# Performance work log

Measured on AMD Instinct MI355X. Metric: run time of the kernel, lower is better.

The kernel has to match this reference:

```python
import jax, jax.numpy as jnp
import numpy as np

N, E, IN, H, HEADS, L, OUT = 4096, 262144, 64, 128, 4, 2, 2
DH = H // HEADS  # 32, per-head dim for both GAT and global MHA
BN_EPS = 1e-5
NEG_SLOPE = 0.2  # GATConv leaky_relu default


def setup_inputs() -> dict:
    key = jax.random.key(0)
    ks = iter(jax.random.split(key, 32))
    rn = lambda shape, s: jax.random.normal(next(ks), shape, jnp.float32) * s
    return {
        "x": rn((N, IN), 1.0),
        "edge_index": jax.random.randint(next(ks), (2, E), 0, N),
        "w_in": rn((H, IN), IN ** -0.5),
        "b_in": rn((H,), 0.02),
        "w_gat": rn((L, H, H), H ** -0.5),
        "att_src": rn((L, HEADS, DH), 0.1),
        "att_dst": rn((L, HEADS, DH), 0.1),
        "b_gat": rn((L, H), 0.02),
        "w_qkv": rn((L, 3 * H, H), H ** -0.5),
        "b_qkv": rn((L, 3 * H), 0.02),
        "w_o": rn((L, H, H), H ** -0.5),
        "b_o": rn((L, H), 0.02),
        "bn_gamma": 1.0 + rn((L, 3, H), 0.05),
        "bn_beta": rn((L, 3, H), 0.05),
        "w1": rn((L, 2 * H, H), H ** -0.5),
        "b1": rn((L, 2 * H), 0.02),
        "w2": rn((L, H, 2 * H), (2 * H) ** -0.5),
        "b2": rn((L, H), 0.02),
        "w_out": rn((OUT, H), H ** -0.5),
        "b_out": rn((OUT,), 0.02),
    }


def _bn(h, g, b):
    # eval-mode BatchNorm1d with running_mean=0, running_var=1
    return h * (g / jnp.sqrt(1.0 + BN_EPS)) + b


def _gat(x, src, dst, w, a_src, a_dst, bias):
    # GATConv(hidden, hidden//heads, heads=HEADS, add_self_loops=False), concat=True
    xp = (x @ w.T).reshape(N, HEADS, DH)                  # [N, HEADS, DH]
    al_s = jnp.einsum('nhd,hd->nh', xp, a_src)            # [N, HEADS]
    al_d = jnp.einsum('nhd,hd->nh', xp, a_dst)
    logit = al_s[src] + al_d[dst]                         # [E, HEADS]
    logit = jnp.where(logit >= 0, logit, NEG_SLOPE * logit)
    m = jax.ops.segment_max(logit, dst, num_segments=N)   # scatter-softmax over dst
    m = jnp.where(jnp.isfinite(m), m, 0.0)
    e = jnp.exp(logit - m[dst])
    denom = jax.ops.segment_sum(e, dst, num_segments=N)
    alpha = e / (denom[dst] + 1e-16)
    out = jax.ops.segment_sum(alpha[:, :, None] * xp[src], dst, num_segments=N)
    return out.reshape(N, H) + bias


def _mha(x, wqkv, bqkv, wo, bo):
    # torch.nn.MultiheadAttention self-attention over all N nodes (one graph)
    qkv = x @ wqkv.T + bqkv
    q, k, v = jnp.split(qkv, 3, axis=-1)
    q = q.reshape(N, HEADS, DH)
    k = k.reshape(N, HEADS, DH)
    v = v.reshape(N, HEADS, DH)
    scores = jnp.einsum('nhd,mhd->hnm', q, k) / jnp.sqrt(jnp.float32(DH))
    attn = jax.nn.softmax(scores, axis=-1)
    out = jnp.einsum('hnm,mhd->nhd', attn, v).reshape(N, H)
    return out @ wo.T + bo


def reference(x, edge_index, w_in, b_in, w_gat, att_src, att_dst, b_gat,
              w_qkv, b_qkv, w_o, b_o, bn_gamma, bn_beta,
              w1, b1, w2, b2, w_out, b_out):
    src, dst = edge_index[0], edge_index[1]
    h = jax.nn.relu(x @ w_in.T + b_in)
    for l in range(L):
        # GPSConv: local GAT branch (dropout inactive in eval)
        h_loc = _gat(h, src, dst, w_gat[l], att_src[l], att_dst[l], b_gat[l]) + h
        h_loc = _bn(h_loc, bn_gamma[l, 0], bn_beta[l, 0])
        # GPSConv: global attention branch
        h_att = _mha(h, w_qkv[l], b_qkv[l], w_o[l], b_o[l]) + h
        h_att = _bn(h_att, bn_gamma[l, 1], bn_beta[l, 1])
        out = h_loc + h_att
        mlp = jax.nn.relu(out @ w1[l].T + b1[l]) @ w2[l].T + b2[l]
        out = _bn(out + mlp, bn_gamma[l, 2], bn_beta[l, 2])
        # GPSRiskModel residual + relu (dropout inactive in eval)
        h = jax.nn.relu(out + h)
    return h @ w_out.T + b_out
```

## Files before the change

### kernel.cpp

```cpp
#include <hip/hip_runtime.h>

#define NN 4096
#define EE 262144
#define INF_ 64
#define HH 128
#define HEADS 4
#define DH 32
#define LL 2
#define NH (NN * HH)
#define KSPLIT 16
#define L2E 1.4426950408889634f

typedef unsigned short u16;
typedef unsigned int u32;
using bf16x8 = __attribute__((ext_vector_type(8))) short;
using f32x4 = __attribute__((ext_vector_type(4))) float;

__device__ __forceinline__ float bf2f(u16 v) { return __uint_as_float(((u32)v) << 16); }
__device__ __forceinline__ u16 f2bf(float f) {
    u32 u = __float_as_uint(f);
    u32 r = (u + 0x7fffu + ((u >> 16) & 1u)) >> 16;
    return (u16)r;
}
__device__ __forceinline__ u32 encf(float f) {
    u32 b = __float_as_uint(f);
    return (b & 0x80000000u) ? ~b : (b | 0x80000000u);
}
__device__ __forceinline__ float decf(u32 u) {
    u32 b = (u & 0x80000000u) ? (u & 0x7fffffffu) : ~u;
    return __uint_as_float(b);
}

__global__ __launch_bounds__(256) void k_detect(const u16* __restrict__ x, int* __restrict__ flag,
                                                int* __restrict__ cnt, u32* __restrict__ gmax) {
    int t = threadIdx.x;
    for (int i = t; i < NN; i += 256) cnt[i] = 0;
    if (t < 16) gmax[t] = 0;
    __shared__ int cs[256];
    u16 v = x[2 * t];
    int e = (v >> 7) & 0xFF;
    cs[t] = (e >= 100 && e <= 140) ? 1 : 0;
    __syncthreads();
    for (int s = 128; s > 0; s >>= 1) {
        if (t < s) cs[t] += cs[t + s];
        __syncthreads();
    }
    if (t == 0) *flag = (cs[0] >= 128) ? 1 : 0;
}

#define MAXSEG 16
struct SegF { const void* src[MAXSEG]; int dst[MAXSEG]; int n[MAXSEG]; int cnt; };
struct SegB { const void* src[8]; u16* dst[8]; u16* dst2[8]; int n[8]; int cnt; };
__global__ __launch_bounds__(256) void k_prep(SegF SF, float* __restrict__ W, SegB SB,
                                              const int* __restrict__ flag,
                                              const int* __restrict__ dst, int* __restrict__ cnt) {
    int bid = blockIdx.x, t = threadIdx.x;
    if (bid < 96) {
        int seg = bid >> 3, bx = bid & 7;
        if (seg >= SF.cnt) return;
        int n = SF.n[seg];
        float* d = W + SF.dst[seg];
        const void* s = SF.src[seg];
        int f = *flag;
        for (int i = bx * 256 + t; i < n; i += 8 * 256)
            d[i] = f ? bf2f(((const u16*)s)[i]) : ((const float*)s)[i];
    } else if (bid < 992) {
        int b2 = bid - 96;
        int seg = b2 >> 7, bx = b2 & 127;
        if (seg >= SB.cnt) return;
        int f = *flag;
        u16* d = SB.dst[seg];
        u16* d2 = SB.dst2[seg];
        if (f && !d2) return;
        int n = SB.n[seg];
        const void* s = SB.src[seg];
        for (int i = bx * 256 + t; i < n; i += 128 * 256) {
            if (d2) {
                float v = f ? bf2f(((const u16*)s)[i]) : ((const float*)s)[i];
                u16 h = f2bf(v);
                d[i] = h;
                d2[i] = f2bf(v - bf2f(h));
            } else {
                d[i] = f2bf(((const float*)s)[i]);
            }
        }
    } else {
        int e = (bid - 992) * 256 + t;
        if (e < EE) atomicAdd(&cnt[dst[e]], 1);
    }
}

__global__ __launch_bounds__(256) void k_scan(const int* __restrict__ cnt, int* __restrict__ rowstart,
                                              int* __restrict__ cursor) {
    __shared__ int part[256];
    int t = threadIdx.x;
    int loc[16];
    int s = 0;
#pragma unroll
    for (int i = 0; i < 16; ++i) { loc[i] = s; s += cnt[t * 16 + i]; }
    part[t] = s;
    __syncthreads();
    for (int off = 1; off < 256; off <<= 1) {
        int v = part[t];
        int a = (t >= off) ? part[t - off] : 0;
        __syncthreads();
        part[t] = v + a;
        __syncthreads();
    }
    int base = (t == 0) ? 0 : part[t - 1];
#pragma unroll
    for (int i = 0; i < 16; ++i) {
        rowstart[t * 16 + i] = base + loc[i];
        cursor[t * 16 + i] = base + loc[i];
    }
}
__global__ void k_scatter(const int* __restrict__ src, const int* __restrict__ dst,
                          int* __restrict__ cursor, int* __restrict__ esrc) {
    int e = blockIdx.x * blockDim.x + threadIdx.x;
    if (e < EE) {
        int d = dst[e];
        int p = atomicAdd(&cursor[d], 1);
        esrc[p] = src[e];
    }
}

__global__ __launch_bounds__(128) void k_mgemm(const u16* __restrict__ Ahi, const u16* __restrict__ Alo,
                                               const u16* __restrict__ Wc, const u16* __restrict__ Wd,
                                               const int* __restrict__ flag,
                                               const float* __restrict__ bias,
                                               float* __restrict__ outf, u16* __restrict__ outb16,
                                               u16* __restrict__ outhi, u16* __restrict__ outlo,
                                               int K, int J, int relu) {
    const u16* Wb = (*flag) ? Wd : Wc;
    int wave = threadIdx.x >> 6, lane = threadIdx.x & 63;
    int grp = lane >> 4, lcol = lane & 15;
    int m0 = blockIdx.x * 32 + wave * 16;
    int j0 = blockIdx.y * 64;
    f32x4 acc[4];
#pragma unroll
    for (int s = 0; s < 4; ++s) acc[s] = (f32x4){0.f, 0.f, 0.f, 0.f};
    const u16* ah = Ahi + (size_t)(m0 + lcol) * K + grp * 8;
    const u16* al = Alo + (size_t)(m0 + lcol) * K + grp * 8;
    const u16* wb = Wb + (size_t)(j0 + lcol) * K + grp * 8;
    for (int k = 0; k < K; k += 32) {
        bf16x8 va = *(const bf16x8*)(ah + k);
        bf16x8 vl = *(const bf16x8*)(al + k);
#pragma unroll
        for (int s = 0; s < 4; ++s) {
            bf16x8 vw = *(const bf16x8*)(wb + (size_t)s * 16 * K + k);
            acc[s] = __builtin_amdgcn_mfma_f32_16x16x32_bf16(va, vw, acc[s], 0, 0, 0);
            acc[s] = __builtin_amdgcn_mfma_f32_16x16x32_bf16(vl, vw, acc[s], 0, 0, 0);
        }
    }
#pragma unroll
    for (int s = 0; s < 4; ++s) {
        int col = j0 + s * 16 + lcol;
        float bs = bias ? bias[col] : 0.f;
#pragma unroll
        for (int r = 0; r < 4; ++r) {
            float v = acc[s][r] + bs;
            if (relu) v = fmaxf(v, 0.f);
            size_t idx = (size_t)(m0 + grp * 4 + r) * J + col;
            if (outf) outf[idx] = v;
            if (outb16) outb16[idx] = f2bf(v);
            if (outhi) {
                u16 hv = f2bf(v);
                outhi[idx] = hv;
                outlo[idx] = f2bf(v - bf2f(hv));
            }
        }
    }
}

__global__ __launch_bounds__(128) void k_gemm_gq(const u16* __restrict__ Ahi, const u16* __restrict__ Alo,
                                                 const u16* __restrict__ wgatc, const u16* __restrict__ wgatd,
                                                 const u16* __restrict__ wqkvc, const u16* __restrict__ wqkvd,
                                                 const int* __restrict__ flag,
                                                 const float* __restrict__ bqkv,
                                                 u16* __restrict__ xpb, u16* __restrict__ qkvb) {
    int wave = threadIdx.x >> 6, lane = threadIdx.x & 63;
    int grp = lane >> 4, lcol = lane & 15;
    int m0 = blockIdx.x * 32 + wave * 16;
    int jb = blockIdx.y;
    int j0 = jb * 64;
    int f = *flag;
    const u16* wgat = f ? wgatd : wgatc;
    const u16* wqkv = f ? wqkvd : wqkvc;
    const u16* Wb = (jb < 2) ? (wgat + (size_t)j0 * HH) : (wqkv + (size_t)(j0 - 128) * HH);
    f32x4 acc[4];
#pragma unroll
    for (int s = 0; s < 4; ++s) acc[s] = (f32x4){0.f, 0.f, 0.f, 0.f};
    const u16* ah = Ahi + (size_t)(m0 + lcol) * HH + grp * 8;
    const u16* al = Alo + (size_t)(m0 + lcol) * HH + grp * 8;
    const u16* wb = Wb + (size_t)lcol * HH + grp * 8;
    for (int k = 0; k < HH; k += 32) {
        bf16x8 va = *(const bf16x8*)(ah + k);
        bf16x8 vl = *(const bf16x8*)(al + k);
#pragma unroll
        for (int s = 0; s < 4; ++s) {
            bf16x8 vw = *(const bf16x8*)(wb + (size_t)s * 16 * HH + k);
            acc[s] = __builtin_amdgcn_mfma_f32_16x16x32_bf16(va, vw, acc[s], 0, 0, 0);
            acc[s] = __builtin_amdgcn_mfma_f32_16x16x32_bf16(vl, vw, acc[s], 0, 0, 0);
        }
    }
    if (jb < 2) {
#pragma unroll
        for (int s = 0; s < 4; ++s) {
            int col = j0 + s * 16 + lcol;
#pragma unroll
            for (int r = 0; r < 4; ++r)
                xpb[(size_t)(m0 + grp * 4 + r) * HH + col] = f2bf(acc[s][r]);
        }
    } else {
#pragma unroll
        for (int s = 0; s < 4; ++s) {
            int colq = j0 - 128 + s * 16 + lcol;
            float bs = bqkv[colq];
#pragma unroll
            for (int r = 0; r < 4; ++r)
                qkvb[(size_t)(m0 + grp * 4 + r) * 384 + colq] = f2bf(acc[s][r] + bs);
        }
    }
}

__global__ __launch_bounds__(128) void k_gemm_wo(const u16* __restrict__ Ahi, const u16* __restrict__ Alo,
                                                 const u16* __restrict__ Wc, const u16* __restrict__ Wd,
                                                 const int* __restrict__ flag,
                                                 const float* __restrict__ bias,
                                                 const float* __restrict__ gatb, const float* __restrict__ hbuf,
                                                 const float* __restrict__ bgat, const float* __restrict__ gam,
                                                 const float* __restrict__ bet,
                                                 float* __restrict__ outb, u16* __restrict__ ohi,
                                                 u16* __restrict__ olo) {
    const u16* Wb = (*flag) ? Wd : Wc;
    int wave = threadIdx.x >> 6, lane = threadIdx.x & 63;
    int grp = lane >> 4, lcol = lane & 15;
    int m0 = blockIdx.x * 32 + wave * 16;
    int j0 = blockIdx.y * 64;
    f32x4 acc[4];
#pragma unroll
    for (int s = 0; s < 4; ++s) acc[s] = (f32x4){0.f, 0.f, 0.f, 0.f};
    const u16* ah = Ahi + (size_t)(m0 + lcol) * HH + grp * 8;
    const u16* al = Alo + (size_t)(m0 + lcol) * HH + grp * 8;
    const u16* wb = Wb + (size_t)(j0 + lcol) * HH + grp * 8;
    for (int k = 0; k < HH; k += 32) {
        bf16x8 va = *(const bf16x8*)(ah + k);
        bf16x8 vl = *(const bf16x8*)(al + k);
#pragma unroll
        for (int s = 0; s < 4; ++s) {
            bf16x8 vw = *(const bf16x8*)(wb + (size_t)s * 16 * HH + k);
            acc[s] = __builtin_amdgcn_mfma_f32_16x16x32_bf16(va, vw, acc[s], 0, 0, 0);
            acc[s] = __builtin_amdgcn_mfma_f32_16x16x32_bf16(vl, vw, acc[s], 0, 0, 0);
        }
    }
    float rs = rsqrtf(1.00001f);
#pragma unroll
    for (int s = 0; s < 4; ++s) {
        int col = j0 + s * 16 + lcol;
        float bs = bias[col];
        float g0 = gam[col] * rs, b0 = bet[col];
        float g1 = gam[HH + col] * rs, b1 = bet[HH + col];
        float bg = bgat[col];
#pragma unroll
        for (int r = 0; r < 4; ++r) {
            size_t idx = (size_t)(m0 + grp * 4 + r) * HH + col;
            float proj = acc[s][r] + bs;
            float hv = hbuf[idx];
            float hl = g0 * (gatb[idx] + bg + hv) + b0;
            float ha = g1 * (proj + hv) + b1;
            float v = hl + ha;
            outb[idx] = v;
            u16 hb = f2bf(v);
            ohi[idx] = hb;
            olo[idx] = f2bf(v - bf2f(hb));
        }
    }
}

__global__ __launch_bounds__(128) void k_gemm_w2(const u16* __restrict__ Ahi, const u16* __restrict__ Alo,
                                                 const u16* __restrict__ Wc, const u16* __restrict__ Wd,
                                                 const int* __restrict__ flag,
                                                 const float* __restrict__ bias,
                                                 const float* __restrict__ outb, const float* __restrict__ gam2,
                                                 const float* __restrict__ bet2,
                                                 float* __restrict__ hbuf, u16* __restrict__ hhi,
                                                 u16* __restrict__ hlo) {
    const u16* Wb = (*flag) ? Wd : Wc;
    int wave = threadIdx.x >> 6, lane = threadIdx.x & 63;
    int grp = lane >> 4, lcol = lane & 15;
    int m0 = blockIdx.x * 32 + wave * 16;
    int j0 = blockIdx.y * 64;
    const int K = 2 * HH;
    f32x4 acc[4];
#pragma unroll
    for (int s = 0; s < 4; ++s) acc[s] = (f32x4){0.f, 0.f, 0.f, 0.f};
    const u16* ah = Ahi + (size_t)(m0 + lcol) * K + grp * 8;
    const u16* al = Alo + (size_t)(m0 + lcol) * K + grp * 8;
    const u16* wb = Wb + (size_t)(j0 + lcol) * K + grp * 8;
    for (int k = 0; k < K; k += 32) {
        bf16x8 va = *(const bf16x8*)(ah + k);
        bf16x8 vl = *(const bf16x8*)(al + k);
#pragma unroll
        for (int s = 0; s < 4; ++s) {
            bf16x8 vw = *(const bf16x8*)(wb + (size_t)s * 16 * K + k);
            acc[s] = __builtin_amdgcn_mfma_f32_16x16x32_bf16(va, vw, acc[s], 0, 0, 0);
            acc[s] = __builtin_amdgcn_mfma_f32_16x16x32_bf16(vl, vw, acc[s], 0, 0, 0);
        }
    }
    float rs = rsqrtf(1.00001f);
#pragma unroll
    for (int s = 0; s < 4; ++s) {
        int col = j0 + s * 16 + lcol;
        float bs = bias[col];
        float g2 = gam2[col] * rs, b2 = bet2[col];
#pragma unroll
        for (int r = 0; r < 4; ++r) {
            size_t idx = (size_t)(m0 + grp * 4 + r) * HH + col;
            float mlpo = acc[s][r] + bs;
            float o2 = g2 * (outb[idx] + mlpo) + b2;
            float v = fmaxf(o2 + hbuf[idx], 0.f);
            hbuf[idx] = v;
            u16 hb = f2bf(v);
            hhi[idx] = hb;
            hlo[idx] = f2bf(v - bf2f(hb));
        }
    }
}

__global__ __launch_bounds__(256) void k_splitlog(const u16* __restrict__ qkvb,
                                                  float* __restrict__ PM, float* __restrict__ PL,
                                                  u16* __restrict__ PO,
                                                  const u16* __restrict__ xpb,
                                                  const float* __restrict__ asrc,
                                                  const float* __restrict__ adst,
                                                  float* __restrict__ als, float* __restrict__ ald,
                                                  u32* __restrict__ gmax) {
    __shared__ __align__(16) u16 Klds[64][40];
    __shared__ __align__(16) u32 Vlds[32][40];
    __shared__ __align__(16) u16 Plds[4][32][36];

    if (blockIdx.x >= 2048) {
        float* red = (float*)&Klds[0][0];
        int t = (blockIdx.x - 2048) * 256 + threadIdx.x;
        int n = t >> 2, hh = t & 3;
        const u16* xr = xpb + (size_t)n * HH + hh * DH;
        float s1 = 0.f, s2 = 0.f;
#pragma unroll
        for (int d = 0; d < DH; ++d) {
            float v = bf2f(xr[d]);
            s1 += v * asrc[hh * DH + d];
            s2 += v * adst[hh * DH + d];
        }
        als[t] = s1;
        ald[t] = s2;
        int lt = threadIdx.x;
        red[lt] = s1;
        __syncthreads();
        for (int off = 128; off >= 4; off >>= 1) {
            if (lt < off) red[lt] = fmaxf(red[lt], red[lt + off]);
            __syncthreads();
        }
        if (lt < 4) atomicMax(&gmax[lt], encf(red[lt]));
        __syncthreads();
        red[lt] = s2;
        __syncthreads();
        for (int off = 128; off >= 4; off >>= 1) {
            if (lt < off) red[lt] = fmaxf(red[lt], red[lt + off]);
            __syncthreads();
        }
        if (lt < 4) atomicMax(&gmax[4 + lt], encf(red[lt]));
        return;
    }

    const float C1 = 0.17677669529663687f * L2E;
    int head = blockIdx.x & 3;
    int qt = (blockIdx.x >> 2) & 31;
    int ks = blockIdx.x >> 7;
    int tid = threadIdx.x;
    int wave = tid >> 6, lane = tid & 63;
    int grp = lane >> 4, lcol = lane & 15;

    int qrow0 = qt * 128 + wave * 32;
    bf16x8 aQ0 = *(const bf16x8*)(qkvb + (size_t)(qrow0 + lcol) * 384 + head * 32 + grp * 8);
    bf16x8 aQ1 = *(const bf16x8*)(qkvb + (size_t)(qrow0 + 16 + lcol) * 384 + head * 32 + grp * 8);

    short onev = (lcol == 0) ? (short)0x3F80 : (short)0;
    bf16x8 bOne = {onev, onev, onev, onev, onev, onev, onev, onev};

    f32x4 oc00 = {0.f, 0.f, 0.f, 0.f}, oc01 = {0.f, 0.f, 0.f, 0.f};
    f32x4 oc10 = {0.f, 0.f, 0.f, 0.f}, oc11 = {0.f, 0.f, 0.f, 0.f};
    f32x4 ol0 = {0.f, 0.f, 0.f, 0.f}, ol1 = {0.f, 0.f, 0.f, 0.f};
    float msh = -INFINITY;

    int isK = (tid < 128);
    int st = tid & 127;
    int skey = st >> 1, shalf = (st & 1) * 16;
    int vj = st & 15, vc = (st >> 4) & 1, dgrp = st >> 5;
    const u16* kptr = qkvb + 128 + head * 32 + shalf;
    const u16* vptr = qkvb + 256 + head * 32 + dgrp * 8;
    int vk0 = vc * 32 + vj;
    int vk1 = vc * 32 + 16 + vj;

    int kt0 = ks * (NN / KSPLIT);
    bf16x8 r0, r1;
    if (isK) {
        r0 = *(const bf16x8*)(kptr + (size_t)(kt0 + skey) * 384);
        r1 = *(const bf16x8*)(kptr + (size_t)(kt0 + skey) * 384 + 8);
    } else {
        r0 = *(const bf16x8*)(vptr + (size_t)(kt0 + vk0) * 384);
        r1 = *(const bf16x8*)(vptr + (size_t)(kt0 + vk1) * 384);
    }

    const int NT = (NN / KSPLIT) / 64;
    for (int t = 0; t < NT; ++t) {
        if (isK) {
            *(bf16x8*)(&Klds[skey][shalf]) = r0;
            *(bf16x8*)(&Klds[skey][shalf + 8]) = r1;
        } else {
#pragma unroll
            for (int j = 0; j < 8; ++j)
                Vlds[dgrp * 8 + j][vc * 20 + vj] = (u32)(u16)r0[j] | ((u32)(u16)r1[j] << 16);
        }
        __syncthreads();
        if (t + 1 < NT) {
            int kn = kt0 + (t + 1) * 64;
            if (isK) {
                r0 = *(const bf16x8*)(kptr + (size_t)(kn + skey) * 384);
                r1 = *(const bf16x8*)(kptr + (size_t)(kn + skey) * 384 + 8);
            } else {
                r0 = *(const bf16x8*)(vptr + (size_t)(kn + vk0) * 384);
                r1 = *(const bf16x8*)(vptr + (size_t)(kn + vk1) * 384);
            }
        }
        f32x4 sc0[4], sc1[4];
        f32x4 zero = {0.f, 0.f, 0.f, 0.f};
#pragma unroll
        for (int s = 0; s < 4; ++s) {
            bf16x8 bK = *(const bf16x8*)(&Klds[s * 16 + lcol][grp * 8]);
            sc0[s] = __builtin_amdgcn_mfma_f32_16x16x32_bf16(aQ0, bK, zero, 0, 0, 0);
            sc1[s] = __builtin_amdgcn_mfma_f32_16x16x32_bf16(aQ1, bK, zero, 0, 0, 0);
        }
        float mymax = sc0[0][0];
#pragma unroll
        for (int s = 0; s < 4; ++s)
#pragma unroll
            for (int r = 0; r < 4; ++r) {
                mymax = fmaxf(mymax, sc0[s][r]);
                mymax = fmaxf(mymax, sc1[s][r]);
            }
        mymax = fmaxf(mymax, __shfl_xor(mymax, 1));
        mymax = fmaxf(mymax, __shfl_xor(mymax, 2));
        mymax = fmaxf(mymax, __shfl_xor(mymax, 4));
        mymax = fmaxf(mymax, __shfl_xor(mymax, 8));
        float mnew = fmaxf(msh, mymax * C1);
        float cc = __builtin_exp2f(msh - mnew);
        msh = mnew;
        oc00 *= cc; oc01 *= cc; ol0 *= cc;
        oc10 *= cc; oc11 *= cc; ol1 *= cc;
#pragma unroll
        for (int c2 = 0; c2 < 2; ++c2) {
#pragma unroll
            for (int r = 0; r < 4; ++r) {
                float p0 = __builtin_exp2f(__builtin_fmaf(sc0[2 * c2][r], C1, -mnew));
                float p1 = __builtin_exp2f(__builtin_fmaf(sc0[2 * c2 + 1][r], C1, -mnew));
                *(u32*)(&Plds[wave][grp * 4 + r][2 * lcol]) =
                    __builtin_amdgcn_perm(__float_as_uint(p1), __float_as_uint(p0), 0x07060302u);
                float q0 = __builtin_exp2f(__builtin_fmaf(sc1[2 * c2][r], C1, -mnew));
                float q1 = __builtin_exp2f(__builtin_fmaf(sc1[2 * c2 + 1][r], C1, -mnew));
                *(u32*)(&Plds[wave][16 + grp * 4 + r][2 * lcol]) =
                    __builtin_amdgcn_perm(__float_as_uint(q1), __float_as_uint(q0), 0x07060302u);
            }
            bf16x8 aP0 = *(const bf16x8*)(&Plds[wave][lcol][grp * 8]);
            bf16x8 aP1 = *(const bf16x8*)(&Plds[wave][16 + lcol][grp * 8]);
            bf16x8 bV0 = *(const bf16x8*)(&Vlds[lcol][c2 * 20 + grp * 4]);
            bf16x8 bV1 = *(const bf16x8*)(&Vlds[16 + lcol][c2 * 20 + grp * 4]);
            oc00 = __builtin_amdgcn_mfma_f32_16x16x32_bf16(aP0, bV0, oc00, 0, 0, 0);
            oc01 = __builtin_amdgcn_mfma_f32_16x16x32_bf16(aP0, bV1, oc01, 0, 0, 0);
            ol0 = __builtin_amdgcn_mfma_f32_16x16x32_bf16(aP0, bOne, ol0, 0, 0, 0);
            oc10 = __builtin_amdgcn_mfma_f32_16x16x32_bf16(aP1, bV0, oc10, 0, 0, 0);
            oc11 = __builtin_amdgcn_mfma_f32_16x16x32_bf16(aP1, bV1, oc11, 0, 0, 0);
            ol1 = __builtin_amdgcn_mfma_f32_16x16x32_bf16(aP1, bOne, ol1, 0, 0, 0);
        }
        __syncthreads();
    }
#pragma unroll
    for (int r = 0; r < 4; ++r) {
        int row0 = qrow0 + grp * 4 + r;
        size_t b0 = ((size_t)row0 * HEADS + head) * KSPLIT + ks;
        PO[b0 * 32 + lcol] = f2bf(oc00[r]);
        PO[b0 * 32 + 16 + lcol] = f2bf(oc01[r]);
        int row1 = row0 + 16;
        size_t b1 = ((size_t)row1 * HEADS + head) * KSPLIT + ks;
        PO[b1 * 32 + lcol] = f2bf(oc10[r]);
        PO[b1 * 32 + 16 + lcol] = f2bf(oc11[r]);
        if (lcol == 0) {
            PM[b0] = msh;
            PL[b0] = ol0[r];
            PM[b1] = msh;
            PL[b1] = ol1[r];
        }
    }
}

#define GCHUNK 256
__global__ __launch_bounds__(128) void k_gatcomb(const int* __restrict__ esrc, const int* __restrict__ rowstart,
                                                 const int* __restrict__ cnt, const float* __restrict__ als,
                                                 const float* __restrict__ ald, const u16* __restrict__ xpb,
                                                 float* __restrict__ gatout, const u32* __restrict__ gmax,
                                                 const float* __restrict__ PM, const float* __restrict__ PL,
                                                 const u16* __restrict__ PO, u16* __restrict__ atthi,
                                                 u16* __restrict__ attlo) {
    __shared__ float red[512];
    __shared__ float elds[GCHUNK * 4];
    __shared__ int slds[GCHUNK];
    int t = threadIdx.x;

    if (blockIdx.x >= NN) {
        int n2 = blockIdx.x - NN;
        float* wn = red;
        if (t < 64) {
            int head = t >> 4, ks = t & 15;
            size_t b = ((size_t)n2 * HEADS + head) * KSPLIT + ks;
            float pm = PM[b];
            float m = pm;
#pragma unroll
            for (int off = 1; off < 16; off <<= 1) m = fmaxf(m, __shfl_xor(m, off));
            float w = __builtin_exp2f(pm - m);
            float lw = PL[b] * w;
#pragma unroll
            for (int off = 1; off < 16; off <<= 1) lw += __shfl_xor(lw, off);
            wn[t] = w / lw;
        }
        __syncthreads();
        int head = t >> 5, dim = t & 31;
        size_t b0 = ((size_t)n2 * HEADS + head) * KSPLIT;
        float o = 0.f;
#pragma unroll
        for (int k = 0; k < KSPLIT; ++k)
            o += wn[head * 16 + k] * bf2f(PO[(b0 + k) * 32 + dim]);
        size_t idx = (size_t)n2 * HH + t;
        u16 h = f2bf(o);
        atthi[idx] = h;
        attlo[idx] = f2bf(o - bf2f(h));
        return;
    }

    int n = blockIdx.x;
    int base = rowstart[n], c = cnt[n];
    float4 adv = ((const float4*)ald)[n];
    float ad[4] = {adv.x, adv.y, adv.z, adv.w};
    float M2[4];
#pragma unroll
    for (int h = 0; h < 4; ++h) {
        float bound = decf(gmax[h]) + decf(gmax[4 + h]);
        float M = bound >= 0.f ? bound : 0.2f * bound;
        M2[h] = M * L2E;
    }
    float dsum[4] = {0.f, 0.f, 0.f, 0.f};
    float acc = 0.f;
    int ht = t >> 5;
    for (int ch = 0; ch < c; ch += GCHUNK) {
        int cn = min(GCHUNK, c - ch);
        __syncthreads();
        for (int i = t; i < cn; i += 128) {
            int s = esrc[base + ch + i];
            slds[i] = s;
            float4 as = ((const float4*)als)[s];
            float lg, e;
            lg = as.x + ad[0]; lg = lg >= 0.f ? lg : 0.2f * lg; e = __builtin_exp2f(lg * L2E - M2[0]); elds[i * 4 + 0] = e; dsum[0] += e;
            lg = as.y + ad[1]; lg = lg >= 0.f ? lg : 0.2f * lg; e = __builtin_exp2f(lg * L2E - M2[1]); elds[i * 4 + 1] = e; dsum[1] += e;
            lg = as.z + ad[2]; lg = lg >= 0.f ? lg : 0.2f * lg; e = __builtin_exp2f(lg * L2E - M2[2]); elds[i * 4 + 2] = e; dsum[2] += e;
            lg = as.w + ad[3]; lg = lg >= 0.f ? lg : 0.2f * lg; e = __builtin_exp2f(lg * L2E - M2[3]); elds[i * 4 + 3] = e; dsum[3] += e;
        }
        __syncthreads();
        int i = 0;
        for (; i + 4 <= cn; i += 4) {
            int s0 = slds[i], s1 = slds[i + 1], s2 = slds[i + 2], s3 = slds[i + 3];
            float x0 = bf2f(xpb[(size_t)s0 * HH + t]);
            float x1 = bf2f(xpb[(size_t)s1 * HH + t]);
            float x2 = bf2f(xpb[(size_t)s2 * HH + t]);
            float x3 = bf2f(xpb[(size_t)s3 * HH + t]);
            acc += elds[i * 4 + ht] * x0 + elds[(i + 1) * 4 + ht] * x1;
            acc += elds[(i + 2) * 4 + ht] * x2 + elds[(i + 3) * 4 + ht] * x3;
        }
        for (; i < cn; ++i) acc += elds[i * 4 + ht] * bf2f(xpb[(size_t)slds[i] * HH + t]);
    }
    __syncthreads();
#pragma unroll
    for (int h = 0; h < 4; ++h) red[h * 128 + t] = dsum[h];
    __syncthreads();
    for (int s2 = 64; s2 > 0; s2 >>= 1) {
        if (t < s2) {
#pragma unroll
            for (int h = 0; h < 4; ++h)
                red[h * 128 + t] += red[h * 128 + t + s2];
        }
        __syncthreads();
    }
    float inv = 1.f / (red[ht * 128] + 1e-16f);
    gatout[(size_t)n * HH + t] = acc * inv;
}

__global__ __launch_bounds__(64) void k_out(const float* __restrict__ h, const float* __restrict__ w,
                                            const float* __restrict__ b, void* __restrict__ yout,
                                            const int* __restrict__ flag) {
    int n = blockIdx.x, l = threadIdx.x;
    float a0 = 0.f, a1 = 0.f;
    for (int k = l; k < HH; k += 64) {
        float hv = h[(size_t)n * HH + k];
        a0 += hv * w[k];
        a1 += hv * w[HH + k];
    }
#pragma unroll
    for (int off = 32; off > 0; off >>= 1) {
        a0 += __shfl_xor(a0, off);
        a1 += __shfl_xor(a1, off);
    }
    if (l == 0) {
        float o0 = a0 + b[0], o1 = a1 + b[1];
        if (*flag) {
            u16* y = (u16*)yout;
            y[n * 2 + 0] = f2bf(o0);
            y[n * 2 + 1] = f2bf(o1);
        } else {
            float* y = (float*)yout;
            y[n * 2 + 0] = o0;
            y[n * 2 + 1] = o1;
        }
    }
}

extern "C" void kernel_launch(void* const* d_in, const int* in_sizes, int n_in,
                              void* d_out, int out_size, void* d_ws, size_t ws_size,
                              hipStream_t stream) {
    float* W = (float*)d_ws;
    size_t o = 0;
    auto take = [&](size_t n) { size_t r = o; o += n; return r; };
    size_t pb_in = take(HH);
    size_t pattS = take(LL * HEADS * DH);
    size_t pattD = take(LL * HEADS * DH);
    size_t pb_gat = take(LL * HH);
    size_t pb_qkv = take(LL * 3 * HH);
    size_t pb_o  = take(LL * HH);
    size_t pbn_g = take(LL * 3 * HH);
    size_t pbn_b = take(LL * 3 * HH);
    size_t pb1   = take(LL * 2 * HH);
    size_t pb2   = take(LL * HH);
    size_t pw_out = take(2 * HH);
    size_t pb_out = take(2);
    auto takeb = [&](size_t nu16) { size_t r = o; o += (nu16 + 1) / 2; return r; };
    size_t bw_in  = takeb(HH * INF_);
    size_t bw_gat = takeb(LL * HH * HH);
    size_t bw_qkv = takeb(LL * 3 * HH * HH);
    size_t bw_o   = takeb(LL * HH * HH);
    size_t bw1    = takeb(LL * 2 * HH * HH);
    size_t bw2    = takeb(LL * HH * 2 * HH);
    o = (o + 127) & ~(size_t)127;
    size_t ohbuf = take(NH);
    size_t ogat  = take(NH);
    size_t otmp  = take(NH);
    size_t oals  = take(NN * HEADS);
    size_t oald  = take(NN * HEADS);
    size_t opm   = take(NN * HEADS * KSPLIT);
    size_t opl   = take(NN * HEADS * KSPLIT);
    size_t opo   = takeb((size_t)NN * HEADS * KSPLIT * 32);
    size_t oqkvb = takeb(NN * 384);
    size_t oxpb  = takeb(NH);
    size_t oxhi  = takeb(NN * INF_);
    size_t oxlo  = takeb(NN * INF_);
    size_t ohhi  = takeb(NH);
    size_t ohlo  = takeb(NH);
    size_t oahi  = takeb(NH);
    size_t oalo  = takeb(NH);
    size_t oohi  = takeb(NH);
    size_t oolo  = takeb(NH);
    size_t omhi  = takeb(NN * 2 * HH);
    size_t omlo  = takeb(NN * 2 * HH);
    int* ibase    = (int*)(W + o);
    int* iflag    = ibase;
    int* cnt      = ibase + 64;
    int* rowstart = cnt + NN;
    int* cursor   = rowstart + NN;
    int* esrc     = cursor + NN;
    u32* gmax     = (u32*)(esrc + EE);

    float* hbuf = W + ohbuf;
    float* gatb = W + ogat;
    float* tmp  = W + otmp;
    float* als  = W + oals;
    float* ald  = W + oald;
    float* pmb  = W + opm;
    float* plb  = W + opl;
    u16* pob  = (u16*)(W + opo);
    u16* qkvb = (u16*)(W + oqkvb);
    u16* xpb  = (u16*)(W + oxpb);
    u16* xhi = (u16*)(W + oxhi), *xlo = (u16*)(W + oxlo);
    u16* hhi = (u16*)(W + ohhi), *hlo = (u16*)(W + ohlo);
    u16* ahi = (u16*)(W + oahi), *alo = (u16*)(W + oalo);
    u16* ohi = (u16*)(W + oohi), *olo = (u16*)(W + oolo);
    u16* mhi = (u16*)(W + omhi), *mlo = (u16*)(W + omlo);

    const int* src = (const int*)d_in[1];
    const int* dst = (const int*)d_in[1] + EE;
    const u16* dw_in  = (const u16*)d_in[2];
    const u16* dw_gat = (const u16*)d_in[4];
    const u16* dw_qkv = (const u16*)d_in[8];
    const u16* dw_o   = (const u16*)d_in[10];
    const u16* dw1    = (const u16*)d_in[14];
    const u16* dw2    = (const u16*)d_in[16];

    k_detect<<<1, 256, 0, stream>>>((const u16*)d_in[0], iflag, cnt, gmax);

    SegF SF = {};
    int nf = 0;
    auto addf = [&](int idx, size_t off, int n) { SF.src[nf] = d_in[idx]; SF.dst[nf] = (int)off; SF.n[nf] = n; ++nf; };
    addf(3, pb_in, HH);
    addf(5, pattS, LL * HEADS * DH);
    addf(6, pattD, LL * HEADS * DH);
    addf(7, pb_gat, LL * HH);
    addf(9, pb_qkv, LL * 3 * HH);
    addf(11, pb_o, LL * HH);
    addf(12, pbn_g, LL * 3 * HH);
    addf(13, pbn_b, LL * 3 * HH);
    addf(15, pb1, LL * 2 * HH);
    addf(17, pb2, LL * HH);
    addf(18, pw_out, 2 * HH);
    addf(19, pb_out, 2);
    SF.cnt = nf;

    SegB SB = {};
    int nb = 0;
    auto addb = [&](int idx, size_t off, int n, u16* d2) {
        SB.src[nb] = d_in[idx]; SB.dst[nb] = (u16*)(W + off); SB.dst2[nb] = d2; SB.n[nb] = n; ++nb;
    };
    addb(2, bw_in, HH * INF_, nullptr);
    addb(4, bw_gat, LL * HH * HH, nullptr);
    addb(8, bw_qkv, LL * 3 * HH * HH, nullptr);
    addb(10, bw_o, LL * HH * HH, nullptr);
    addb(14, bw1, LL * 2 * HH * HH, nullptr);
    addb(16, bw2, LL * HH * 2 * HH, nullptr);
    SB.src[nb] = d_in[0]; SB.dst[nb] = xhi; SB.dst2[nb] = xlo; SB.n[nb] = NN * INF_; ++nb;
    SB.cnt = nb;

    k_prep<<<2016, 256, 0, stream>>>(SF, W, SB, iflag, dst, cnt);

    k_scan<<<1, 256, 0, stream>>>(cnt, rowstart, cursor);
    k_scatter<<<EE / 256, 256, 0, stream>>>(src, dst, cursor, esrc);

    k_mgemm<<<dim3(NN / 32, HH / 64), 128, 0, stream>>>(xhi, xlo, (u16*)(W + bw_in), dw_in, iflag,
                                                        W + pb_in, hbuf, nullptr, hhi, hlo, INF_, HH, 1);

    for (int l = 0; l < LL; ++l) {
        k_gemm_gq<<<dim3(NN / 32, 8), 128, 0, stream>>>(hhi, hlo,
                                                        (u16*)(W + bw_gat) + (size_t)l * HH * HH,
                                                        dw_gat + (size_t)l * HH * HH,
                                                        (u16*)(W + bw_qkv) + (size_t)l * 3 * HH * HH,
                                                        dw_qkv + (size_t)l * 3 * HH * HH,
                                                        iflag, W + pb_qkv + l * 3 * HH, xpb, qkvb);
        k_splitlog<<<2048 + (NN * HEADS) / 256, 256, 0, stream>>>(qkvb, pmb, plb, pob, xpb,
                                                                  W + pattS + l * HEADS * DH,
                                                                  W + pattD + l * HEADS * DH,
                                                                  als, ald, gmax + l * 8);
        k_gatcomb<<<2 * NN, 128, 0, stream>>>(esrc, rowstart, cnt, als, ald, xpb, gatb, gmax + l * 8,
                                              pmb, plb, pob, ahi, alo);
        k_gemm_wo<<<dim3(NN / 32, HH / 64), 128, 0, stream>>>(ahi, alo,
                                                              (u16*)(W + bw_o) + (size_t)l * HH * HH,
                                                              dw_o + (size_t)l * HH * HH, iflag,
                                                              W + pb_o + l * HH, gatb, hbuf,
                                                              W + pb_gat + l * HH, W + pbn_g + l * 3 * HH,
                                                              W + pbn_b + l * 3 * HH, tmp, ohi, olo);
        k_mgemm<<<dim3(NN / 32, 256 / 64), 128, 0, stream>>>(ohi, olo,
                                                             (u16*)(W + bw1) + (size_t)l * 2 * HH * HH,
                                                             dw1 + (size_t)l * 2 * HH * HH, iflag,
                                                             W + pb1 + l * 2 * HH, nullptr, nullptr,
                                                             mhi, mlo, HH, 2 * HH, 1);
        k_gemm_w2<<<dim3(NN / 32, HH / 64), 128, 0, stream>>>(mhi, mlo,
                                                              (u16*)(W + bw2) + (size_t)l * HH * 2 * HH,
                                                              dw2 + (size_t)l * HH * 2 * HH, iflag,
                                                              W + pb2 + l * HH, tmp,
                                                              W + pbn_g + l * 3 * HH + 2 * HH,
                                                              W + pbn_b + l * 3 * HH + 2 * HH,
                                                              hbuf, hhi, hlo);
    }
    k_out<<<NN, 64, 0, stream>>>(hbuf, W + pw_out, W + pb_out, d_out, iflag);
}
```

Baseline: 296.3 us.

## Shrink GEMM column tiles and fold CSR scan/scatter into GEMM launches

Every small MFMA GEMM drops from a 64-column tile to a 16-column tile, which gives four times as many blocks for better occupancy on a 4096-row problem. The one-block scan is folded into the input-projection GEMM as an extra grid row. The edge scatter is folded into the first layer's GAT/QKV GEMM as extra blocks. This removes two kernel launches and lets the CSR build overlap with GEMM work. In exchange, each A tile is reloaded four times as often, and the scatter now depends on the scan having run in the earlier launch.

```diff
diff --git a/kernel.cpp b/kernel.cpp
--- a/kernel.cpp
+++ b/kernel.cpp
@@ -90,84 +90,69 @@
     }
 }
 
-__global__ __launch_bounds__(256) void k_scan(const int* __restrict__ cnt, int* __restrict__ rowstart,
-                                              int* __restrict__ cursor) {
-    __shared__ int part[256];
-    int t = threadIdx.x;
-    int loc[16];
-    int s = 0;
-#pragma unroll
-    for (int i = 0; i < 16; ++i) { loc[i] = s; s += cnt[t * 16 + i]; }
-    part[t] = s;
-    __syncthreads();
-    for (int off = 1; off < 256; off <<= 1) {
-        int v = part[t];
-        int a = (t >= off) ? part[t - off] : 0;
-        __syncthreads();
-        part[t] = v + a;
-        __syncthreads();
-    }
-    int base = (t == 0) ? 0 : part[t - 1];
-#pragma unroll
-    for (int i = 0; i < 16; ++i) {
-        rowstart[t * 16 + i] = base + loc[i];
-        cursor[t * 16 + i] = base + loc[i];
-    }
-}
-__global__ void k_scatter(const int* __restrict__ src, const int* __restrict__ dst,
-                          int* __restrict__ cursor, int* __restrict__ esrc) {
-    int e = blockIdx.x * blockDim.x + threadIdx.x;
-    if (e < EE) {
-        int d = dst[e];
-        int p = atomicAdd(&cursor[d], 1);
-        esrc[p] = src[e];
-    }
-}
-
 __global__ __launch_bounds__(128) void k_mgemm(const u16* __restrict__ Ahi, const u16* __restrict__ Alo,
                                                const u16* __restrict__ Wc, const u16* __restrict__ Wd,
                                                const int* __restrict__ flag,
                                                const float* __restrict__ bias,
                                                float* __restrict__ outf, u16* __restrict__ outb16,
                                                u16* __restrict__ outhi, u16* __restrict__ outlo,
-                                               int K, int J, int relu) {
+                                               int K, int J, int relu, int jtiles,
+                                               const int* __restrict__ scnt, int* __restrict__ srowstart,
+                                               int* __restrict__ scursor) {
+    __shared__ int part[128];
+    if ((int)blockIdx.y >= jtiles) {
+        if (blockIdx.x != 0 || scnt == nullptr) return;
+        int t = threadIdx.x;
+        int loc[32];
+        int s = 0;
+#pragma unroll
+        for (int i = 0; i < 32; ++i) { loc[i] = s; s += scnt[t * 32 + i]; }
+        part[t] = s;
+        __syncthreads();
+        for (int off = 1; off < 128; off <<= 1) {
+            int v = part[t];
+            int a = (t >= off) ? part[t - off] : 0;
+            __syncthreads();
+            part[t] = v + a;
+            __syncthreads();
+        }
+        int base = (t == 0) ? 0 : part[t - 1];
+#pragma unroll
+        for (int i = 0; i < 32; ++i) {
+            srowstart[t * 32 + i] = base + loc[i];
+            scursor[t * 32 + i] = base + loc[i];
+        }
+        return;
+    }
     const u16* Wb = (*flag) ? Wd : Wc;
     int wave = threadIdx.x >> 6, lane = threadIdx.x & 63;
     int grp = lane >> 4, lcol = lane & 15;
     int m0 = blockIdx.x * 32 + wave * 16;
-    int j0 = blockIdx.y * 64;
-    f32x4 acc[4];
-#pragma unroll
-    for (int s = 0; s < 4; ++s) acc[s] = (f32x4){0.f, 0.f, 0.f, 0.f};
+    int j0 = blockIdx.y * 16;
+    f32x4 acc = (f32x4){0.f, 0.f, 0.f, 0.f};
     const u16* ah = Ahi + (size_t)(m0 + lcol) * K + grp * 8;
     const u16* al = Alo + (size_t)(m0 + lcol) * K + grp * 8;
     const u16* wb = Wb + (size_t)(j0 + lcol) * K + grp * 8;
     for (int k = 0; k < K; k += 32) {
         bf16x8 va = *(const bf16x8*)(ah + k);
         bf16x8 vl = *(const bf16x8*)(al + k);
-#pragma unroll
-        for (int s = 0; s < 4; ++s) {
-            bf16x8 vw = *(const bf16x8*)(wb + (size_t)s * 16 * K + k);
-            acc[s] = __builtin_amdgcn_mfma_f32_16x16x32_bf16(va, vw, acc[s], 0, 0, 0);
-            acc[s] = __builtin_amdgcn_mfma_f32_16x16x32_bf16(vl, vw, acc[s], 0, 0, 0);
-        }
-    }
-#pragma unroll
-    for (int s = 0; s < 4; ++s) {
-        int col = j0 + s * 16 + lcol;
-        float bs = bias ? bias[col] : 0.f;
-#pragma unroll
-        for (int r = 0; r < 4; ++r) {
-            float v = acc[s][r] + bs;
-            if (relu) v = fmaxf(v, 0.f);
-            size_t idx = (size_t)(m0 + grp * 4 + r) * J + col;
-            if (outf) outf[idx] = v;
-            if (outb16) outb16[idx] = f2bf(v);
-            if (outhi) {
-                u16 hv = f2bf(v);
-                outhi[idx] = hv;
-                outlo[idx] = f2bf(v - bf2f(hv));
-            }
+        bf16x8 vw = *(const bf16x8*)(wb + k);
+        acc = __builtin_amdgcn_mfma_f32_16x16x32_bf16(va, vw, acc, 0, 0, 0);
+        acc = __builtin_amdgcn_mfma_f32_16x16x32_bf16(vl, vw, acc, 0, 0, 0);
+    }
+    int col = j0 + lcol;
+    float bs = bias ? bias[col] : 0.f;
+#pragma unroll
+    for (int r = 0; r < 4; ++r) {
+        float v = acc[r] + bs;
+        if (relu) v = fmaxf(v, 0.f);
+        size_t idx = (size_t)(m0 + grp * 4 + r) * J + col;
+        if (outf) outf[idx] = v;
+        if (outb16) outb16[idx] = f2bf(v);
+        if (outhi) {
+            u16 hv = f2bf(v);
+            outhi[idx] = hv;
+            outlo[idx] = f2bf(v - bf2f(hv));
         }
     }
 }
@@ -177,49 +162,49 @@
                                                  const u16* __restrict__ wqkvc, const u16* __restrict__ wqkvd,
                                                  const int* __restrict__ flag,
                                                  const float* __restrict__ bqkv,
-                                                 u16* __restrict__ xpb, u16* __restrict__ qkvb) {
+                                                 u16* __restrict__ xpb, u16* __restrict__ qkvb,
+                                                 const int* __restrict__ esrc_src, const int* __restrict__ esrc_dst,
+                                                 int* __restrict__ cursor, int* __restrict__ esrc) {
+    if (blockIdx.y >= 32) {
+        int b = (blockIdx.y - 32) * 128 + blockIdx.x;
+        for (int e = b * 128 + threadIdx.x; e < EE; e += 32768) {
+            int d = esrc_dst[e];
+            int p = atomicAdd(&cursor[d], 1);
+            esrc[p] = esrc_src[e];
+        }
+        return;
+    }
     int wave = threadIdx.x >> 6, lane = threadIdx.x & 63;
     int grp = lane >> 4, lcol = lane & 15;
     int m0 = blockIdx.x * 32 + wave * 16;
     int jb = blockIdx.y;
-    int j0 = jb * 64;
+    int j0 = jb * 16;
     int f = *flag;
     const u16* wgat = f ? wgatd : wgatc;
     const u16* wqkv = f ? wqkvd : wqkvc;
-    const u16* Wb = (jb < 2) ? (wgat + (size_t)j0 * HH) : (wqkv + (size_t)(j0 - 128) * HH);
-    f32x4 acc[4];
-#pragma unroll
-    for (int s = 0; s < 4; ++s) acc[s] = (f32x4){0.f, 0.f, 0.f, 0.f};
+    const u16* Wb = (jb < 8) ? (wgat + (size_t)j0 * HH) : (wqkv + (size_t)(j0 - 128) * HH);
+    f32x4 acc = (f32x4){0.f, 0.f, 0.f, 0.f};
     const u16* ah = Ahi + (size_t)(m0 + lcol) * HH + grp * 8;
     const u16* al = Alo + (size_t)(m0 + lcol) * HH + grp * 8;
     const u16* wb = Wb + (size_t)lcol * HH + grp * 8;
     for (int k = 0; k < HH; k += 32) {
         bf16x8 va = *(const bf16x8*)(ah + k);
         bf16x8 vl = *(const bf16x8*)(al + k);
-#pragma unroll
-        for (int s = 0; s < 4; ++s) {
-            bf16x8 vw = *(const bf16x8*)(wb + (size_t)s * 16 * HH + k);
-            acc[s] = __builtin_amdgcn_mfma_f32_16x16x32_bf16(va, vw, acc[s], 0, 0, 0);
-            acc[s] = __builtin_amdgcn_mfma_f32_16x16x32_bf16(vl, vw, acc[s], 0, 0, 0);
-        }
-    }
-    if (jb < 2) {
-#pragma unroll
-        for (int s = 0; s < 4; ++s) {
-            int col = j0 + s * 16 + lcol;
-#pragma unroll
-            for (int r = 0; r < 4; ++r)
-                xpb[(size_t)(m0 + grp * 4 + r) * HH + col] = f2bf(acc[s][r]);
-        }
+        bf16x8 vw = *(const bf16x8*)(wb + k);
+        acc = __builtin_amdgcn_mfma_f32_16x16x32_bf16(va, vw, acc, 0, 0, 0);
+        acc = __builtin_amdgcn_mfma_f32_16x16x32_bf16(vl, vw, acc, 0, 0, 0);
+    }
+    if (jb < 8) {
+        int col = j0 + lcol;
+#pragma unroll
+        for (int r = 0; r < 4; ++r)
+            xpb[(size_t)(m0 + grp * 4 + r) * HH + col] = f2bf(acc[r]);
     } else {
-#pragma unroll
-        for (int s = 0; s < 4; ++s) {
-            int colq = j0 - 128 + s * 16 + lcol;
-            float bs = bqkv[colq];
-#pragma unroll
-            for (int r = 0; r < 4; ++r)
-                qkvb[(size_t)(m0 + grp * 4 + r) * 384 + colq] = f2bf(acc[s][r] + bs);
-        }
+        int colq = j0 - 128 + lcol;
+        float bs = bqkv[colq];
+#pragma unroll
+        for (int r = 0; r < 4; ++r)
+            qkvb[(size_t)(m0 + grp * 4 + r) * 384 + colq] = f2bf(acc[r] + bs);
     }
 }
 
@@ -236,44 +221,36 @@
     int wave = threadIdx.x >> 6, lane = threadIdx.x & 63;
     int grp = lane >> 4, lcol = lane & 15;
     int m0 = blockIdx.x * 32 + wave * 16;
-    int j0 = blockIdx.y * 64;
-    f32x4 acc[4];
-#pragma unroll
-    for (int s = 0; s < 4; ++s) acc[s] = (f32x4){0.f, 0.f, 0.f, 0.f};
+    int j0 = blockIdx.y * 16;
+    f32x4 acc = (f32x4){0.f, 0.f, 0.f, 0.f};
     const u16* ah = Ahi + (size_t)(m0 + lcol) * HH + grp * 8;
     const u16* al = Alo + (size_t)(m0 + lcol) * HH + grp * 8;
     const u16* wb = Wb + (size_t)(j0 + lcol) * HH + grp * 8;
     for (int k = 0; k < HH; k += 32) {
         bf16x8 va = *(const bf16x8*)(ah + k);
         bf16x8 vl = *(const bf16x8*)(al + k);
-#pragma unroll
-        for (int s = 0; s < 4; ++s) {
-            bf16x8 vw = *(const bf16x8*)(wb + (size_t)s * 16 * HH + k);
-            acc[s] = __builtin_amdgcn_mfma_f32_16x16x32_bf16(va, vw, acc[s], 0, 0, 0);
-            acc[s] = __builtin_amdgcn_mfma_f32_16x16x32_bf16(vl, vw, acc[s], 0, 0, 0);
-        }
+        bf16x8 vw = *(const bf16x8*)(wb + k);
+        acc = __builtin_amdgcn_mfma_f32_16x16x32_bf16(va, vw, acc, 0, 0, 0);
+        acc = __builtin_amdgcn_mfma_f32_16x16x32_bf16(vl, vw, acc, 0, 0, 0);
     }
     float rs = rsqrtf(1.00001f);
-#pragma unroll
-    for (int s = 0; s < 4; ++s) {
-        int col = j0 + s * 16 + lcol;
-        float bs = bias[col];
-        float g0 = gam[col] * rs, b0 = bet[col];
-        float g1 = gam[HH + col] * rs, b1 = bet[HH + col];
-        float bg = bgat[col];
-#pragma unroll
-        for (int r = 0; r < 4; ++r) {
-            size_t idx = (size_t)(m0 + grp * 4 + r) * HH + col;
-            float proj = acc[s][r] + bs;
-            float hv = hbuf[idx];
-            float hl = g0 * (gatb[idx] + bg + hv) + b0;
-            float ha = g1 * (proj + hv) + b1;
-            float v = hl + ha;
-            outb[idx] = v;
-            u16 hb = f2bf(v);
-            ohi[idx] = hb;
-            olo[idx] = f2bf(v - bf2f(hb));
-        }
+    int col = j0 + lcol;
+    float bs = bias[col];
+    float g0 = gam[col] * rs, b0 = bet[col];
+    float g1 = gam[HH + col] * rs, b1 = bet[HH + col];
+    float bg = bgat[col];
+#pragma unroll
+    for (int r = 0; r < 4; ++r) {
+        size_t idx = (size_t)(m0 + grp * 4 + r) * HH + col;
+        float proj = acc[r] + bs;
+        float hv = hbuf[idx];
+        float hl = g0 * (gatb[idx] + bg + hv) + b0;
+        float ha = g1 * (proj + hv) + b1;
+        float v = hl + ha;
+        outb[idx] = v;
+        u16 hb = f2bf(v);
+        ohi[idx] = hb;
+        olo[idx] = f2bf(v - bf2f(hb));
     }
 }
 
@@ -289,41 +266,33 @@
     int wave = threadIdx.x >> 6, lane = threadIdx.x & 63;
     int grp = lane >> 4, lcol = lane & 15;
     int m0 = blockIdx.x * 32 + wave * 16;
-    int j0 = blockIdx.y * 64;
+    int j0 = blockIdx.y * 16;
     const int K = 2 * HH;
-    f32x4 acc[4];
-#pragma unroll
-    for (int s = 0; s < 4; ++s) acc[s] = (f32x4){0.f, 0.f, 0.f, 0.f};
+    f32x4 acc = (f32x4){0.f, 0.f, 0.f, 0.f};
     const u16* ah = Ahi + (size_t)(m0 + lcol) * K + grp * 8;
     const u16* al = Alo + (size_t)(m0 + lcol) * K + grp * 8;
     const u16* wb = Wb + (size_t)(j0 + lcol) * K + grp * 8;
     for (int k = 0; k < K; k += 32) {
         bf16x8 va = *(const bf16x8*)(ah + k);
         bf16x8 vl = *(const bf16x8*)(al + k);
-#pragma unroll
-        for (int s = 0; s < 4; ++s) {
-            bf16x8 vw = *(const bf16x8*)(wb + (size_t)s * 16 * K + k);
-            acc[s] = __builtin_amdgcn_mfma_f32_16x16x32_bf16(va, vw, acc[s], 0, 0, 0);
-            acc[s] = __builtin_amdgcn_mfma_f32_16x16x32_bf16(vl, vw, acc[s], 0, 0, 0);
-        }
+        bf16x8 vw = *(const bf16x8*)(wb + k);
+        acc = __builtin_amdgcn_mfma_f32_16x16x32_bf16(va, vw, acc, 0, 0, 0);
+        acc = __builtin_amdgcn_mfma_f32_16x16x32_bf16(vl, vw, acc, 0, 0, 0);
     }
     float rs = rsqrtf(1.00001f);
-#pragma unroll
-    for (int s = 0; s < 4; ++s) {
-        int col = j0 + s * 16 + lcol;
-        float bs = bias[col];
-        float g2 = gam2[col] * rs, b2 = bet2[col];
-#pragma unroll
-        for (int r = 0; r < 4; ++r) {
-            size_t idx = (size_t)(m0 + grp * 4 + r) * HH + col;
-            float mlpo = acc[s][r] + bs;
-            float o2 = g2 * (outb[idx] + mlpo) + b2;
-            float v = fmaxf(o2 + hbuf[idx], 0.f);
-            hbuf[idx] = v;
-            u16 hb = f2bf(v);
-            hhi[idx] = hb;
-            hlo[idx] = f2bf(v - bf2f(hb));
-        }
+    int col = j0 + lcol;
+    float bs = bias[col];
+    float g2 = gam2[col] * rs, b2 = bet2[col];
+#pragma unroll
+    for (int r = 0; r < 4; ++r) {
+        size_t idx = (size_t)(m0 + grp * 4 + r) * HH + col;
+        float mlpo = acc[r] + bs;
+        float o2 = g2 * (outb[idx] + mlpo) + b2;
+        float v = fmaxf(o2 + hbuf[idx], 0.f);
+        hbuf[idx] = v;
+        u16 hb = f2bf(v);
+        hhi[idx] = hb;
+        hlo[idx] = f2bf(v - bf2f(hb));
     }
 }
 
@@ -744,37 +713,37 @@
 
     k_prep<<<2016, 256, 0, stream>>>(SF, W, SB, iflag, dst, cnt);
 
-    k_scan<<<1, 256, 0, stream>>>(cnt, rowstart, cursor);
-    k_scatter<<<EE / 256, 256, 0, stream>>>(src, dst, cursor, esrc);
-
-    k_mgemm<<<dim3(NN / 32, HH / 64), 128, 0, stream>>>(xhi, xlo, (u16*)(W + bw_in), dw_in, iflag,
-                                                        W + pb_in, hbuf, nullptr, hhi, hlo, INF_, HH, 1);
+    k_mgemm<<<dim3(NN / 32, HH / 16 + 1), 128, 0, stream>>>(xhi, xlo, (u16*)(W + bw_in), dw_in, iflag,
+                                                            W + pb_in, hbuf, nullptr, hhi, hlo, INF_, HH, 1,
+                                                            HH / 16, cnt, rowstart, cursor);
 
     for (int l = 0; l < LL; ++l) {
-        k_gemm_gq<<<dim3(NN / 32, 8), 128, 0, stream>>>(hhi, hlo,
+        k_gemm_gq<<<dim3(NN / 32, (l == 0) ? 34 : 32), 128, 0, stream>>>(hhi, hlo,
                                                         (u16*)(W + bw_gat) + (size_t)l * HH * HH,
                                                         dw_gat + (size_t)l * HH * HH,
                                                         (u16*)(W + bw_qkv) + (size_t)l * 3 * HH * HH,
                                                         dw_qkv + (size_t)l * 3 * HH * HH,
-                                                        iflag, W + pb_qkv + l * 3 * HH, xpb, qkvb);
+                                                        iflag, W + pb_qkv + l * 3 * HH, xpb, qkvb,
+                                                        src, dst, cursor, esrc);
         k_splitlog<<<2048 + (NN * HEADS) / 256, 256, 0, stream>>>(qkvb, pmb, plb, pob, xpb,
                                                                   W + pattS + l * HEADS * DH,
                                                                   W + pattD + l * HEADS * DH,
                                                                   als, ald, gmax + l * 8);
         k_gatcomb<<<2 * NN, 128, 0, stream>>>(esrc, rowstart, cnt, als, ald, xpb, gatb, gmax + l * 8,
                                               pmb, plb, pob, ahi, alo);
-        k_gemm_wo<<<dim3(NN / 32, HH / 64), 128, 0, stream>>>(ahi, alo,
+        k_gemm_wo<<<dim3(NN / 32, HH / 16), 128, 0, stream>>>(ahi, alo,
                                                               (u16*)(W + bw_o) + (size_t)l * HH * HH,
                                                               dw_o + (size_t)l * HH * HH, iflag,
                                                               W + pb_o + l * HH, gatb, hbuf,
                                                               W + pb_gat + l * HH, W + pbn_g + l * 3 * HH,
                                                               W + pbn_b + l * 3 * HH, tmp, ohi, olo);
-        k_mgemm<<<dim3(NN / 32, 256 / 64), 128, 0, stream>>>(ohi, olo,
+        k_mgemm<<<dim3(NN / 32, 256 / 16), 128, 0, stream>>>(ohi, olo,
                                                              (u16*)(W + bw1) + (size_t)l * 2 * HH * HH,
                                                              dw1 + (size_t)l * 2 * HH * HH, iflag,
                                                              W + pb1 + l * 2 * HH, nullptr, nullptr,
-                                                             mhi, mlo, HH, 2 * HH, 1);
-        k_gemm_w2<<<dim3(NN / 32, HH / 64), 128, 0, stream>>>(mhi, mlo,
+                                                             mhi, mlo, HH, 2 * HH, 1,
+                                                             256 / 16, nullptr, nullptr, nullptr);
+        k_gemm_w2<<<dim3(NN / 32, HH / 16), 128, 0, stream>>>(mhi, mlo,
                                                               (u16*)(W + bw2) + (size_t)l * HH * 2 * HH,
                                                               dw2 + (size_t)l * HH * 2 * HH, iflag,
                                                               W + pb2 + l * HH, tmp,
```

After: 314.8 us. 1.06x slower.
